# Performance work log

Hardware: AMD Instinct MI355X
Metric: run time of the kernel (lower is better)

## Reference

```python
import math
import jax, jax.numpy as jnp
import numpy as np

N_HEADS = 16
THETA = 10000.0


def _rope_cos_sin(S, head_dim):
    half = head_dim // 2
    inv_freq = 1.0 / (THETA ** (jnp.arange(half, dtype=jnp.float32) / half))
    t = jnp.arange(S, dtype=jnp.float32)
    freqs = t[:, None] * inv_freq[None, :]  # [S, half]
    return jnp.cos(freqs), jnp.sin(freqs)


def _apply_rope(x, cos, sin):
    # x: [B, H, S, D] float32; cos/sin: [S, D//2]
    half = x.shape[-1] // 2
    x1, x2 = x[..., :half], x[..., half:]
    c = cos[None, None, :, :]
    s = sin[None, None, :, :]
    return jnp.concatenate([x1 * c - x2 * s, x1 * s + x2 * c], axis=-1)


def setup_inputs() -> dict:
    key = jax.random.key(0)
    k1, k2, k3 = jax.random.split(key, 3)
    B, S, D = 4, 2048, 1024
    x = jax.random.normal(k1, (B, S, D), dtype=jnp.float32)
    w_qkv = jax.random.normal(k2, (3 * D, D), dtype=jnp.float32) * (1.0 / math.sqrt(D))
    w_out = jax.random.normal(k3, (D, D), dtype=jnp.float32) * (1.0 / math.sqrt(D))
    return {"x": x, "w_qkv": w_qkv, "w_out": w_out}


def reference(x, w_qkv, w_out):
    B, S, D = x.shape
    H = N_HEADS
    hd = D // H

    qkv = x @ w_qkv.T  # [B, S, 3D]
    q, k, v = jnp.split(qkv, 3, axis=-1)

    def reshape(t):
        return t.reshape(B, S, H, hd).transpose(0, 2, 1, 3)  # [B,H,S,hd]

    q, k, v = reshape(q), reshape(k), reshape(v)

    cos, sin = _rope_cos_sin(S, hd)
    q = _apply_rope(q.astype(jnp.float32), cos, sin).astype(x.dtype)
    k = _apply_rope(k.astype(jnp.float32), cos, sin).astype(x.dtype)

    scale = math.sqrt(hd)
    scores = jnp.einsum("bhsd,bhtd->bhst", q, k) / scale  # [B,H,S,S]
    causal = jnp.tril(jnp.ones((S, S), dtype=bool))
    scores = jnp.where(causal[None, None], scores, -jnp.inf)
    attn = jax.nn.softmax(scores.astype(jnp.float32), axis=-1).astype(x.dtype)

    out = jnp.einsum("bhst,bhtd->bhsd", attn, v)  # [B,H,S,hd]
    out = out.transpose(0, 2, 1, 3).reshape(B, S, D)
    return out @ w_out.T
```

## Files before the change

kernel.cpp:

```cpp
#include <hip/hip_runtime.h>
#include <hip/hip_bf16.h>

#define DEV static __device__ __forceinline__

typedef unsigned short u16;
typedef unsigned int u32;
typedef __attribute__((ext_vector_type(8))) short short8;
typedef __attribute__((ext_vector_type(4))) float f32x4;
typedef __attribute__((ext_vector_type(16))) float f32x16;
typedef __attribute__((ext_vector_type(4))) u32 u32x4;

static constexpr int Bsz = 4, Ssz = 2048, Dsz = 1024, Hn = 16, HD = 64;
static constexpr int Mrows = Bsz * Ssz;

DEV u16 f2bu(float f) {
  union { float f; u32 u; } a; a.f = f;
  u32 u = a.u;
  u32 r = (u + 0x7FFFu + ((u >> 16) & 1u)) >> 16;
  return (u16)r;
}
DEV float b2f(u16 v) {
  union { u32 u; float f; } a; a.u = ((u32)v) << 16;
  return a.f;
}
DEV u32 pk2(float lo, float hi2) {
  __hip_bfloat162 t = __float22bfloat162_rn(make_float2(lo, hi2));
  u32 r; __builtin_memcpy(&r, &t, 4); return r;
}
DEV f32x16 mfma3232(short8 a, short8 b, f32x16 c) {
  return __builtin_amdgcn_mfma_f32_32x32x16_bf16(a, b, c, 0, 0, 0);
}
DEV float ex2(float x) { return __builtin_amdgcn_exp2f(x); }

__global__ void k_prep(const float4* __restrict__ s0, ushort4* __restrict__ d0, int n0,
                       const float4* __restrict__ s1, ushort4* __restrict__ d1, int n1,
                       const float4* __restrict__ s2, ushort4* __restrict__ d2, int n2,
                       float2* __restrict__ cst) {
  const int stride = gridDim.x * blockDim.x;
  const int ncast = n0 + n1 + n2;
  const int total = ncast + Ssz * 32;
  for (int i = blockIdx.x * blockDim.x + threadIdx.x; i < total; i += stride) {
    if (i < ncast) {
      const float4* s; ushort4* d; int k;
      if (i < n0) { s = s0; d = d0; k = i; }
      else if (i < n0 + n1) { s = s1; d = d1; k = i - n0; }
      else { s = s2; d = d2; k = i - n0 - n1; }
      float4 v = s[k];
      ushort4 o;
      o.x = f2bu(v.x); o.y = f2bu(v.y); o.z = f2bu(v.z); o.w = f2bu(v.w);
      d[k] = o;
    } else {
      const int k = i - ncast;
      const int s = k >> 5, dd = k & 31;
      const float inv = powf(10000.0f, -(float)dd / 32.0f);
      const float fr = (float)s * inv;
      cst[k] = make_float2(cosf(fr), sinf(fr));
    }
  }
}

DEV void cp16(const u16* g, u16* l) {
  __builtin_amdgcn_global_load_lds((const __attribute__((address_space(1))) u32*)g,
                                   (__attribute__((address_space(3))) u32*)l, 16, 0, 0);
}

template <bool OUTBF16>
__global__ __launch_bounds__(256, 2) void k_gemm(const u16* __restrict__ A,
                                                 const u16* __restrict__ W,
                                                 void* __restrict__ C, int N, int K,
                                                 const float2* __restrict__ cst, int cpx,
                                                 u16* __restrict__ vtp) {
  __shared__ __align__(16) u16 SMEM[33792];
  const int tid = threadIdx.x;
  const int wid = tid >> 6, lane = tid & 63;
  const int lr = lane & 15, u = lane >> 4;
  const int wm = wid >> 1, wn = wid & 1;

  const int wg = blockIdx.x;
  const int xcd = wg & 7;
  const int j = wg >> 3;
  const int brow = (j / cpx) * 128;
  const int bcol = (xcd * cpx + j % cpx) * 128;

  const int rw = wid * 32 + (lane >> 3);
  const int octS = ((lane & 7) ^ (rw & 7)) * 8;
  const u16* aS = A + (size_t)(brow + rw) * K + octS;
  const u16* bS = W + (size_t)(bcol + rw) * K + octS;
  const int dBase = wid * 2048 + lane * 8;

  const int aBase = (wm * 64 + lr) * 64;
  const int bBase = (wn * 64 + lr) * 64;
  const int o0 = (u ^ (lane & 7)) * 8;
  const int o1 = ((4 + u) ^ (lane & 7)) * 8;

  f32x4 acc[4][4];
#pragma unroll
  for (int i = 0; i < 4; ++i)
#pragma unroll
    for (int j2 = 0; j2 < 4; ++j2) acc[i][j2] = (f32x4){0.f, 0.f, 0.f, 0.f};

  const int nt = K >> 6;

#define STG(kk, bb)                                                    \
  do {                                                                 \
    u16* ad = SMEM + (bb)*8192 + dBase;                                \
    u16* bd = SMEM + 16384 + (bb)*8192 + dBase;                        \
    cp16(aS + (kk), ad);                                               \
    cp16(aS + (size_t)8 * K + (kk), ad + 512);                         \
    cp16(aS + (size_t)16 * K + (kk), ad + 1024);                       \
    cp16(aS + (size_t)24 * K + (kk), ad + 1536);                       \
    cp16(bS + (kk), bd);                                               \
    cp16(bS + (size_t)8 * K + (kk), bd + 512);                         \
    cp16(bS + (size_t)16 * K + (kk), bd + 1024);                       \
    cp16(bS + (size_t)24 * K + (kk), bd + 1536);                       \
  } while (0)

  STG(0, 0);

  for (int t = 0; t < nt; ++t) {
    asm volatile("s_waitcnt vmcnt(0)" ::: "memory");
    __builtin_amdgcn_s_barrier();
    if (t + 1 < nt) STG((t + 1) << 6, (t + 1) & 1);
    const u16* ab = SMEM + (t & 1) * 8192;
    const u16* bb = SMEM + 16384 + (t & 1) * 8192;
    short8 a0[4], a1[4], b0[4], b1[4];
#pragma unroll
    for (int mr = 0; mr < 4; ++mr) {
      a0[mr] = *(const short8*)(ab + aBase + mr * 1024 + o0);
      a1[mr] = *(const short8*)(ab + aBase + mr * 1024 + o1);
    }
#pragma unroll
    for (int nr = 0; nr < 4; ++nr) {
      b0[nr] = *(const short8*)(bb + bBase + nr * 1024 + o0);
      b1[nr] = *(const short8*)(bb + bBase + nr * 1024 + o1);
    }
    __builtin_amdgcn_s_setprio(1);
#pragma unroll
    for (int mr = 0; mr < 4; ++mr)
#pragma unroll
      for (int nr = 0; nr < 4; ++nr)
        acc[mr][nr] =
            __builtin_amdgcn_mfma_f32_16x16x32_bf16(a0[mr], b0[nr], acc[mr][nr], 0, 0, 0);
#pragma unroll
    for (int mr = 0; mr < 4; ++mr)
#pragma unroll
      for (int nr = 0; nr < 4; ++nr)
        acc[mr][nr] =
            __builtin_amdgcn_mfma_f32_16x16x32_bf16(a1[mr], b1[nr], acc[mr][nr], 0, 0, 0);
    __builtin_amdgcn_s_setprio(0);
  }
#undef STG

  if (OUTBF16) {
    __syncthreads();
    const int rmode = (bcol < 1024) ? 0 : (bcol < 2048) ? 1 : 2;
    if (rmode < 2) {
      const float sc = (rmode == 0) ? 0.18033688f : 1.0f;
#pragma unroll
      for (int mr = 0; mr < 4; ++mr)
#pragma unroll
        for (int r = 0; r < 4; ++r) {
          const int row = wm * 64 + mr * 16 + u * 4 + r;
          const int s = (brow + row) & 2047;
          const float2 c0 = cst[s * 32 + lr];
          const float2 c1 = cst[s * 32 + 16 + lr];
          const float x10 = acc[mr][0][r], x11 = acc[mr][1][r];
          const float x20 = acc[mr][2][r], x21 = acc[mr][3][r];
          u16* lp = SMEM + row * 136 + wn * 64 + lr;
          lp[0]  = f2bu((x10 * c0.x - x20 * c0.y) * sc);
          lp[16] = f2bu((x11 * c1.x - x21 * c1.y) * sc);
          lp[32] = f2bu((x10 * c0.y + x20 * c0.x) * sc);
          lp[48] = f2bu((x11 * c1.y + x21 * c1.x) * sc);
        }
      __syncthreads();
      u16* cp = (u16*)C;
#pragma unroll
      for (int i = 0; i < 8; ++i) {
        const int e = i * 2048 + tid * 8;
        const int row = e >> 7, col = e & 127;
        short8 v = *(const short8*)(SMEM + row * 136 + col);
        *(short8*)(cp + (size_t)(brow + row) * N + bcol + col) = v;
      }
    } else {
#pragma unroll
      for (int mr = 0; mr < 4; ++mr)
#pragma unroll
        for (int nr = 0; nr < 4; ++nr)
#pragma unroll
          for (int r = 0; r < 4; ++r) {
            const int dl = wn * 64 + nr * 16 + lr;
            const int sl = wm * 64 + mr * 16 + u * 4 + r;
            SMEM[dl * 136 + sl] = f2bu(acc[mr][nr][r]);
          }
      __syncthreads();
      const int bb2 = brow >> 11;
      const int sbase = brow & 2047;
#pragma unroll
      for (int i = 0; i < 8; ++i) {
        const int e = i * 2048 + tid * 8;
        const int dl = e >> 7, sl = e & 127;
        const int gd = (bcol - 2048) + dl;
        short8 v = *(const short8*)(SMEM + dl * 136 + sl);
        *(short8*)(vtp + (size_t)(bb2 * 1024 + gd) * 2048 + sbase + sl) = v;
      }
    }
  } else {
    __syncthreads();
    float* FS = (float*)SMEM;
#pragma unroll
    for (int mr = 0; mr < 4; ++mr)
#pragma unroll
      for (int nr = 0; nr < 4; ++nr)
#pragma unroll
        for (int r = 0; r < 4; ++r)
          FS[(wm * 64 + mr * 16 + u * 4 + r) * 132 + wn * 64 + nr * 16 + lr] =
              acc[mr][nr][r];
    __syncthreads();
    float* cp = (float*)C;
#pragma unroll
    for (int i = 0; i < 16; ++i) {
      const int e = i * 1024 + tid * 4;
      const int row = e >> 7, col = e & 127;
      float4 v = *(const float4*)(FS + row * 132 + col);
      *(float4*)(cp + (size_t)(brow + row) * N + bcol + col) = v;
    }
  }
}

__global__ __launch_bounds__(256, 4) void k_attn(const u16* __restrict__ qkv,
                                                 const u16* __restrict__ vt,
                                                 u16* __restrict__ obuf) {
  __shared__ __align__(16) u16 Ksm[2][64 * 64];
  __shared__ __align__(16) u16 Vsm[2][64 * 64];

  const int tid = threadIdx.x;
  const int wid = tid >> 6;
  const int lane = tid & 63;
  const int l31 = lane & 31;
  const int hi = lane >> 5;
  const int r7 = l31 & 7;

  const int fid = blockIdx.x;
  const int a = fid & 3, bq = (fid >> 8) & 3;
  const int bh = (fid >> 2) & 63;
  const int sel = a ^ bq;
  const int qt = (sel == 0) ? bq : (sel == 1) ? 7 - bq : (sel == 2) ? 8 + bq : 15 - bq;

  const int b = bh >> 4;
  const int h = bh & 15;

  const float NEG = -__builtin_inff();

  const int srow = lane >> 3;
  const int scol = ((lane & 7) ^ srow) * 8;
  const u16* ksrc0 = qkv + (size_t)(b * Ssz + wid * 16 + srow) * 3072 + 1024 + h * 64 + scol;
  const u16* ksrc1 = ksrc0 + (size_t)8 * 3072;
  const u16* vsrc0 = vt + ((size_t)bh * 64 + wid * 16 + srow) * Ssz + scol;
  const u16* vsrc1 = vsrc0 + (size_t)8 * Ssz;
  u16* kD0 = Ksm[0] + wid * 1024;
  u16* vD0 = Vsm[0] + wid * 1024;

  const int q0 = qt * 128;
  const int qrow = q0 + (wid << 5) + l31;

  const u16* qptr = qkv + (size_t)(b * Ssz + qrow) * 3072 + h * 64 + hi * 8;
  short8 qf[4];
#pragma unroll
  for (int s = 0; s < 4; ++s) qf[s] = *(const short8*)(qptr + s * 16);

  f32x16 o0 = {0.f}, o1 = {0.f};
  float lsum = 0.f;

  const int ntiles = 2 * qt + 2;
  const int lastT = 2 * qt + (wid >> 1);

  cp16(ksrc0, kD0);
  cp16(ksrc1, kD0 + 512);
  cp16(vsrc0, vD0);
  cp16(vsrc1, vD0 + 512);

  const u16* kS0 = ksrc0 + (size_t)64 * 3072;
  const u16* kS1 = ksrc1 + (size_t)64 * 3072;
  const u16* vS0 = vsrc0 + 64;
  const u16* vS1 = vsrc1 + 64;

  for (int t = 0; t < ntiles; ++t) {
    __syncthreads();
    if (t + 1 < ntiles) {
      const int nb = (t + 1) & 1;
      cp16(kS0, kD0 + nb * 4096);
      cp16(kS1, kD0 + nb * 4096 + 512);
      cp16(vS0, vD0 + nb * 4096);
      cp16(vS1, vD0 + nb * 4096 + 512);
      kS0 += (size_t)64 * 3072;
      kS1 += (size_t)64 * 3072;
      vS0 += 64;
      vS1 += 64;
    }
    if (t > lastT) continue;

    const u16* kbuf = Ksm[t & 1];
    const u16* vbuf = Vsm[t & 1];
    const int kv0 = t << 6;

    f32x16 st0 = {0.f}, st1 = {0.f};
    __builtin_amdgcn_s_setprio(1);
#pragma unroll
    for (int s = 0; s < 4; ++s) {
      const int slot = (((2 * s + hi) ^ r7) << 3);
      short8 k0 = *(const short8*)(kbuf + l31 * 64 + slot);
      short8 k1 = *(const short8*)(kbuf + (32 + l31) * 64 + slot);
      st0 = mfma3232(k0, qf[s], st0);
      st1 = mfma3232(k1, qf[s], st1);
    }
    __builtin_amdgcn_s_setprio(0);

    if (t == lastT) {
      const int kb0 = kv0 + 4 * hi;
#pragma unroll
      for (int r = 0; r < 16; ++r) {
        const int ko = (r & 3) + 8 * (r >> 2);
        if (kb0 + ko > qrow) st0[r] = NEG;
        if (kb0 + 32 + ko > qrow) st1[r] = NEG;
      }
    }

    float rsp[4] = {0.f, 0.f, 0.f, 0.f};
#pragma unroll
    for (int r = 0; r < 16; ++r) {
      const float p0 = ex2(st0[r]);
      const float p1 = ex2(st1[r]);
      st0[r] = p0;
      st1[r] = p1;
      rsp[r & 3] += p0 + p1;
    }
    lsum += (rsp[0] + rsp[1]) + (rsp[2] + rsp[3]);

    u32 wa[8], wb[8];
#pragma unroll
    for (int g = 0; g < 4; ++g) {
      wa[g] = pk2(st0[4 * g + 0], st0[4 * g + 1]);
      wb[g] = pk2(st0[4 * g + 2], st0[4 * g + 3]);
      wa[4 + g] = pk2(st1[4 * g + 0], st1[4 * g + 1]);
      wb[4 + g] = pk2(st1[4 * g + 2], st1[4 * g + 3]);
    }

#pragma unroll
    for (int s = 0; s < 4; ++s) {
      const u32 uA0 = wa[2 * s], uA1 = wa[2 * s + 1];
      const u32 uB0 = wb[2 * s], uB1 = wb[2 * s + 1];
      const u32 tA0 = __shfl_xor(uA0, 32), tA1 = __shfl_xor(uA1, 32);
      const u32 tB0 = __shfl_xor(uB0, 32), tB1 = __shfl_xor(uB1, 32);
      u32x4 pw;
      pw.x = hi ? tA1 : uA0;
      pw.y = hi ? tB1 : uB0;
      pw.z = hi ? uA1 : tA0;
      pw.w = hi ? uB1 : tB0;
      short8 pfrag = *(short8*)&pw;
      const int slot = (((2 * s + hi) ^ r7) << 3);
      short8 v0 = *(const short8*)(vbuf + l31 * 64 + slot);
      short8 v1 = *(const short8*)(vbuf + (32 + l31) * 64 + slot);
      __builtin_amdgcn_s_setprio(1);
      o0 = mfma3232(v0, pfrag, o0);
      o1 = mfma3232(v1, pfrag, o1);
      __builtin_amdgcn_s_setprio(0);
    }
  }

  const float lt = lsum + __shfl_xor(lsum, 32);
  const float inv = 1.0f / lt;
  u16* orow = obuf + (size_t)(b * Ssz + qrow) * 1024 + h * 64;
#pragma unroll
  for (int j = 0; j < 4; ++j) {
    ushort4 s0, s1;
    s0.x = f2bu(o0[4 * j + 0] * inv);
    s0.y = f2bu(o0[4 * j + 1] * inv);
    s0.z = f2bu(o0[4 * j + 2] * inv);
    s0.w = f2bu(o0[4 * j + 3] * inv);
    s1.x = f2bu(o1[4 * j + 0] * inv);
    s1.y = f2bu(o1[4 * j + 1] * inv);
    s1.z = f2bu(o1[4 * j + 2] * inv);
    s1.w = f2bu(o1[4 * j + 3] * inv);
    *(ushort4*)(orow + 8 * j + 4 * hi) = s0;
    *(ushort4*)(orow + 32 + 8 * j + 4 * hi) = s1;
  }
}

extern "C" void kernel_launch(void* const* d_in, const int* in_sizes, int n_in,
                              void* d_out, int out_size, void* d_ws, size_t ws_size,
                              hipStream_t stream) {
  const float* x = (const float*)d_in[0];
  const float* wqkv = (const float*)d_in[1];
  const float* wout = (const float*)d_in[2];

  char* ws = (char*)d_ws;
  u16* xb      = (u16*)(ws + 0);
  u16* wqkvb   = (u16*)(ws + 16777216);
  u16* woutb   = (u16*)(ws + 23068672);
  u16* qkv     = (u16*)(ws + 25165824);
  u16* vt      = (u16*)(ws + 75497472);
  u16* obuf    = (u16*)(ws + 92274688);
  float2* cst  = (float2*)(ws + 109051904);

  k_prep<<<2048, 256, 0, stream>>>(
      (const float4*)x, (ushort4*)xb, Mrows * Dsz / 4,
      (const float4*)wqkv, (ushort4*)wqkvb, 3 * Dsz * Dsz / 4,
      (const float4*)wout, (ushort4*)woutb, Dsz * Dsz / 4, cst);

  k_gemm<true><<<1536, 256, 0, stream>>>(xb, wqkvb, qkv, 3072, 1024, cst, 3, vt);

  k_attn<<<1024, 256, 0, stream>>>(qkv, vt, obuf);

  k_gemm<false><<<512, 256, 0, stream>>>(obuf, woutb, d_out, 1024, 1024, nullptr, 1, nullptr);
}
```

Before: 168.4 us.

## Rewrite GEMM as 256x128 tile, 8-wave, triple-buffered pipeline with interleaved staging

Replaces the 128x128, 4-wave, double-buffered GEMM with 512-thread blocks computing 256x128 tiles. K-tiles are staged through a 3-deep LDS ring two steps ahead, with partial vmcnt waits. Loads are interleaved between four per-column MFMA phases separated by barriers. The aim is to hide global-load latency, share B tiles across more rows and cut synchronisation stalls, at the cost of more LDS per block (lower occupancy), more barriers and epilogue changes for the taller tile.

```diff
diff --git a/kernel.cpp b/kernel.cpp
--- a/kernel.cpp
+++ b/kernel.cpp
@@ -29,6 +29,9 @@
 }
 DEV f32x16 mfma3232(short8 a, short8 b, f32x16 c) {
   return __builtin_amdgcn_mfma_f32_32x32x16_bf16(a, b, c, 0, 0, 0);
+}
+DEV f32x4 mfma16(short8 a, short8 b, f32x4 c) {
+  return __builtin_amdgcn_mfma_f32_16x16x32_bf16(a, b, c, 0, 0, 0);
 }
 DEV float ex2(float x) { return __builtin_amdgcn_exp2f(x); }
 
@@ -65,33 +68,40 @@
 }
 
 template <bool OUTBF16>
-__global__ __launch_bounds__(256, 2) void k_gemm(const u16* __restrict__ A,
-                                                 const u16* __restrict__ W,
-                                                 void* __restrict__ C, int N, int K,
-                                                 const float2* __restrict__ cst, int cpx,
-                                                 u16* __restrict__ vtp) {
-  __shared__ __align__(16) u16 SMEM[33792];
+__global__ __launch_bounds__(512, 2) void k_gemm2(const u16* __restrict__ A,
+                                                  const u16* __restrict__ W,
+                                                  void* __restrict__ C, int N, int K,
+                                                  const float2* __restrict__ cst, int cpx,
+                                                  u16* __restrict__ vtp) {
+  __shared__ __align__(16) u16 SMEM[73728];
   const int tid = threadIdx.x;
   const int wid = tid >> 6, lane = tid & 63;
   const int lr = lane & 15, u = lane >> 4;
+  const int x7 = lane & 7;
   const int wm = wid >> 1, wn = wid & 1;
 
   const int wg = blockIdx.x;
   const int xcd = wg & 7;
-  const int j = wg >> 3;
-  const int brow = (j / cpx) * 128;
-  const int bcol = (xcd * cpx + j % cpx) * 128;
-
-  const int rw = wid * 32 + (lane >> 3);
-  const int octS = ((lane & 7) ^ (rw & 7)) * 8;
-  const u16* aS = A + (size_t)(brow + rw) * K + octS;
-  const u16* bS = W + (size_t)(bcol + rw) * K + octS;
-  const int dBase = wid * 2048 + lane * 8;
-
-  const int aBase = (wm * 64 + lr) * 64;
-  const int bBase = (wn * 64 + lr) * 64;
-  const int o0 = (u ^ (lane & 7)) * 8;
-  const int o1 = ((4 + u) ^ (lane & 7)) * 8;
+  const int jj = wg >> 3;
+  const int brow = (jj / cpx) * 256;
+  const int bcol = (xcd * cpx + jj % cpx) * 128;
+
+  const int rw = tid >> 3;
+  const int octS = ((tid & 7) ^ (rw & 7)) * 8;
+  const u16* aS0 = A + (size_t)(brow + rw) * K + octS;
+  const u16* aS1 = A + (size_t)(brow + 128 + rw) * K + octS;
+  const u16* bS  = W + (size_t)(bcol + rw) * K + octS;
+  const int dOff = tid * 8;
+
+#define STGU(ps, pd, ko)                          \
+  do {                                            \
+    cp16((ps) + (ko), (pd));                      \
+    cp16((ps) + (size_t)64 * K + (ko), (pd) + 4096); \
+  } while (0)
+
+  const int arow = (wm & 1) * 64 + lr;
+  const u16* AhB = SMEM + (wm >> 1) * 8192;
+  const int brih = wn * 64 + lr;
 
   f32x4 acc[4][4];
 #pragma unroll
@@ -99,57 +109,61 @@
 #pragma unroll
     for (int j2 = 0; j2 < 4; ++j2) acc[i][j2] = (f32x4){0.f, 0.f, 0.f, 0.f};
 
-  const int nt = K >> 6;
-
-#define STG(kk, bb)                                                    \
-  do {                                                                 \
-    u16* ad = SMEM + (bb)*8192 + dBase;                                \
-    u16* bd = SMEM + 16384 + (bb)*8192 + dBase;                        \
-    cp16(aS + (kk), ad);                                               \
-    cp16(aS + (size_t)8 * K + (kk), ad + 512);                         \
-    cp16(aS + (size_t)16 * K + (kk), ad + 1024);                       \
-    cp16(aS + (size_t)24 * K + (kk), ad + 1536);                       \
-    cp16(bS + (kk), bd);                                               \
-    cp16(bS + (size_t)8 * K + (kk), bd + 512);                         \
-    cp16(bS + (size_t)16 * K + (kk), bd + 1024);                       \
-    cp16(bS + (size_t)24 * K + (kk), bd + 1536);                       \
-  } while (0)
-
-  STG(0, 0);
-
-  for (int t = 0; t < nt; ++t) {
-    asm volatile("s_waitcnt vmcnt(0)" ::: "memory");
+  const int KT = K >> 6;
+
+  STGU(aS0, SMEM + dOff, 0);
+  STGU(aS1, SMEM + 8192 + dOff, 0);
+  STGU(bS, SMEM + 49152 + dOff, 0);
+  STGU(aS0, SMEM + 16384 + dOff, 64);
+  STGU(aS1, SMEM + 24576 + dOff, 64);
+  STGU(bS, SMEM + 57344 + dOff, 64);
+
+#define PHASE(nc)                                                     \
+  {                                                                   \
+    const u16* br = Bb + (brih + (nc) * 16) * 64;                     \
+    short8 b0 = *(const short8*)(br + (u ^ x7) * 8);                  \
+    short8 b1 = *(const short8*)(br + ((4 + u) ^ x7) * 8);            \
+    asm volatile("s_barrier" ::: "memory");                           \
+    __builtin_amdgcn_s_setprio(1);                                    \
+    _Pragma("unroll") for (int mr = 0; mr < 4; ++mr) {                \
+      acc[mr][(nc)] = mfma16(af0[mr], b0, acc[mr][(nc)]);             \
+      acc[mr][(nc)] = mfma16(af1[mr], b1, acc[mr][(nc)]);             \
+    }                                                                 \
+    __builtin_amdgcn_s_setprio(0);                                    \
+    asm volatile("s_barrier" ::: "memory");                           \
+  }
+
+  int buf = 0, sbuf = 2;
+  for (int kt = 0; kt < KT; ++kt) {
+    if (kt + 1 < KT) asm volatile("s_waitcnt vmcnt(6)" ::: "memory");
+    else             asm volatile("s_waitcnt vmcnt(0)" ::: "memory");
     __builtin_amdgcn_s_barrier();
-    if (t + 1 < nt) STG((t + 1) << 6, (t + 1) & 1);
-    const u16* ab = SMEM + (t & 1) * 8192;
-    const u16* bb = SMEM + 16384 + (t & 1) * 8192;
-    short8 a0[4], a1[4], b0[4], b1[4];
+    const u16* Ah = AhB + buf * 16384;
+    const u16* Bb = SMEM + 49152 + buf * 8192;
+    const bool dost = (kt + 2 < KT);
+    const int k2 = (kt + 2) << 6;
+    u16* sA = SMEM + sbuf * 16384 + dOff;
+    u16* sB = SMEM + 49152 + sbuf * 8192 + dOff;
+
+    short8 af0[4], af1[4];
+    if (dost) STGU(aS0, sA, k2);
 #pragma unroll
     for (int mr = 0; mr < 4; ++mr) {
-      a0[mr] = *(const short8*)(ab + aBase + mr * 1024 + o0);
-      a1[mr] = *(const short8*)(ab + aBase + mr * 1024 + o1);
-    }
-#pragma unroll
-    for (int nr = 0; nr < 4; ++nr) {
-      b0[nr] = *(const short8*)(bb + bBase + nr * 1024 + o0);
-      b1[nr] = *(const short8*)(bb + bBase + nr * 1024 + o1);
-    }
-    __builtin_amdgcn_s_setprio(1);
-#pragma unroll
-    for (int mr = 0; mr < 4; ++mr)
-#pragma unroll
-      for (int nr = 0; nr < 4; ++nr)
-        acc[mr][nr] =
-            __builtin_amdgcn_mfma_f32_16x16x32_bf16(a0[mr], b0[nr], acc[mr][nr], 0, 0, 0);
-#pragma unroll
-    for (int mr = 0; mr < 4; ++mr)
-#pragma unroll
-      for (int nr = 0; nr < 4; ++nr)
-        acc[mr][nr] =
-            __builtin_amdgcn_mfma_f32_16x16x32_bf16(a1[mr], b1[nr], acc[mr][nr], 0, 0, 0);
-    __builtin_amdgcn_s_setprio(0);
-  }
-#undef STG
+      const u16* ar = Ah + (arow + mr * 16) * 64;
+      af0[mr] = *(const short8*)(ar + (u ^ x7) * 8);
+      af1[mr] = *(const short8*)(ar + ((4 + u) ^ x7) * 8);
+    }
+    PHASE(0)
+    if (dost) STGU(aS1, sA + 8192, k2);
+    PHASE(1)
+    if (dost) STGU(bS, sB, k2);
+    PHASE(2)
+    PHASE(3)
+    buf = (buf == 2) ? 0 : buf + 1;
+    sbuf = (sbuf == 2) ? 0 : sbuf + 1;
+  }
+#undef PHASE
+#undef STGU
 
   if (OUTBF16) {
     __syncthreads();
@@ -159,13 +173,13 @@
 #pragma unroll
       for (int mr = 0; mr < 4; ++mr)
 #pragma unroll
-        for (int r = 0; r < 4; ++r) {
-          const int row = wm * 64 + mr * 16 + u * 4 + r;
+        for (int rr = 0; rr < 4; ++rr) {
+          const int row = wm * 64 + mr * 16 + u * 4 + rr;
           const int s = (brow + row) & 2047;
           const float2 c0 = cst[s * 32 + lr];
           const float2 c1 = cst[s * 32 + 16 + lr];
-          const float x10 = acc[mr][0][r], x11 = acc[mr][1][r];
-          const float x20 = acc[mr][2][r], x21 = acc[mr][3][r];
+          const float x10 = acc[mr][0][rr], x11 = acc[mr][1][rr];
+          const float x20 = acc[mr][2][rr], x21 = acc[mr][3][rr];
           u16* lp = SMEM + row * 136 + wn * 64 + lr;
           lp[0]  = f2bu((x10 * c0.x - x20 * c0.y) * sc);
           lp[16] = f2bu((x11 * c1.x - x21 * c1.y) * sc);
@@ -176,7 +190,7 @@
       u16* cp = (u16*)C;
 #pragma unroll
       for (int i = 0; i < 8; ++i) {
-        const int e = i * 2048 + tid * 8;
+        const int e = i * 4096 + tid * 8;
         const int row = e >> 7, col = e & 127;
         short8 v = *(const short8*)(SMEM + row * 136 + col);
         *(short8*)(cp + (size_t)(brow + row) * N + bcol + col) = v;
@@ -185,44 +199,48 @@
 #pragma unroll
       for (int mr = 0; mr < 4; ++mr)
 #pragma unroll
-        for (int nr = 0; nr < 4; ++nr)
-#pragma unroll
-          for (int r = 0; r < 4; ++r) {
-            const int dl = wn * 64 + nr * 16 + lr;
-            const int sl = wm * 64 + mr * 16 + u * 4 + r;
-            SMEM[dl * 136 + sl] = f2bu(acc[mr][nr][r]);
+        for (int j2 = 0; j2 < 4; ++j2)
+#pragma unroll
+          for (int rr = 0; rr < 4; ++rr) {
+            const int dl = wn * 64 + j2 * 16 + lr;
+            const int sl = wm * 64 + mr * 16 + u * 4 + rr;
+            SMEM[dl * 264 + sl] = f2bu(acc[mr][j2][rr]);
           }
       __syncthreads();
       const int bb2 = brow >> 11;
       const int sbase = brow & 2047;
 #pragma unroll
       for (int i = 0; i < 8; ++i) {
-        const int e = i * 2048 + tid * 8;
-        const int dl = e >> 7, sl = e & 127;
-        const int gd = (bcol - 2048) + dl;
-        short8 v = *(const short8*)(SMEM + dl * 136 + sl);
-        *(short8*)(vtp + (size_t)(bb2 * 1024 + gd) * 2048 + sbase + sl) = v;
+        const int e = i * 4096 + tid * 8;
+        const int dl = e >> 8, sl = e & 255;
+        short8 v = *(const short8*)(SMEM + dl * 264 + sl);
+        *(short8*)(vtp + (size_t)(bb2 * 1024 + (bcol - 2048) + dl) * 2048 + sbase + sl) = v;
       }
     }
   } else {
-    __syncthreads();
     float* FS = (float*)SMEM;
 #pragma unroll
-    for (int mr = 0; mr < 4; ++mr)
-#pragma unroll
-      for (int nr = 0; nr < 4; ++nr)
-#pragma unroll
-        for (int r = 0; r < 4; ++r)
-          FS[(wm * 64 + mr * 16 + u * 4 + r) * 132 + wn * 64 + nr * 16 + lr] =
-              acc[mr][nr][r];
-    __syncthreads();
-    float* cp = (float*)C;
-#pragma unroll
-    for (int i = 0; i < 16; ++i) {
-      const int e = i * 1024 + tid * 4;
-      const int row = e >> 7, col = e & 127;
-      float4 v = *(const float4*)(FS + row * 132 + col);
-      *(float4*)(cp + (size_t)(brow + row) * N + bcol + col) = v;
+    for (int hh = 0; hh < 2; ++hh) {
+      __syncthreads();
+      if ((wm >> 1) == hh) {
+#pragma unroll
+        for (int mr = 0; mr < 4; ++mr)
+#pragma unroll
+          for (int j2 = 0; j2 < 4; ++j2)
+#pragma unroll
+            for (int rr = 0; rr < 4; ++rr)
+              FS[((wm & 1) * 64 + mr * 16 + u * 4 + rr) * 132 + wn * 64 + j2 * 16 + lr] =
+                  acc[mr][j2][rr];
+      }
+      __syncthreads();
+      float* cp = (float*)C;
+#pragma unroll
+      for (int i = 0; i < 8; ++i) {
+        const int e = i * 2048 + tid * 4;
+        const int row = e >> 7, col = e & 127;
+        float4 v = *(const float4*)(FS + row * 132 + col);
+        *(float4*)(cp + (size_t)(brow + hh * 128 + row) * N + bcol + col) = v;
+      }
     }
   }
 }
@@ -407,9 +425,9 @@
       (const float4*)wqkv, (ushort4*)wqkvb, 3 * Dsz * Dsz / 4,
       (const float4*)wout, (ushort4*)woutb, Dsz * Dsz / 4, cst);
 
-  k_gemm<true><<<1536, 256, 0, stream>>>(xb, wqkvb, qkv, 3072, 1024, cst, 3, vt);
+  k_gemm2<true><<<768, 512, 0, stream>>>(xb, wqkvb, qkv, 3072, 1024, cst, 3, vt);
 
   k_attn<<<1024, 256, 0, stream>>>(qkv, vt, obuf);
 
-  k_gemm<false><<<512, 256, 0, stream>>>(obuf, woutb, d_out, 1024, 1024, nullptr, 1, nullptr);
-}
+  k_gemm2<false><<<256, 512, 0, stream>>>(obuf, woutb, d_out, 1024, 1024, nullptr, 1, nullptr);
+}
```

Result: no change. 171.1 us (+1.6%).
